# Kernel tuning notes

Measured on AMD Instinct MI355X. Metric: run time of the kernel, lower is better.

Reference implementation:

```python
import jax, jax.numpy as jnp
from jax import lax
import numpy as np


def _conv4d(x, w, b, stride, padding):
    # Faithful 4D conv emulation: K temporal slices, each its own 3D conv.
    # x: [B,Ci,T,D,H,W]; w: [K,Co,Ci,k,k,k]; b: [K,Co] or None.
    # Quirk preserved: bias b[i] is added once per contributing temporal tap i
    # (the torch code accumulates full conv3d outputs including bias).
    B, Ci, T = x.shape[0], x.shape[1], x.shape[2]
    K = w.shape[0]
    O = (T + 2 * padding - K) // stride + 1
    out = None
    for i in range(K):
        j = np.arange(O) * stride + i - padding          # static input frame idx per output frame
        valid = (j >= 0) & (j < T)
        jc = np.clip(j, 0, T - 1)
        xg = jnp.moveaxis(x[:, :, jc], 2, 1)             # [B,O,Ci,D,H,W]
        xg = xg.reshape(B * O, Ci, x.shape[3], x.shape[4], x.shape[5])
        y = lax.conv_general_dilated(xg, w[i], (stride,) * 3, [(padding, padding)] * 3,
                                     dimension_numbers=('NCDHW', 'OIDHW', 'NCDHW'))
        if b is not None:
            y = y + b[i][None, :, None, None, None]
        y = y.reshape(B, O, y.shape[1], y.shape[2], y.shape[3], y.shape[4])
        y = y * jnp.asarray(valid, y.dtype)[None, :, None, None, None, None]
        out = y if out is None else out + y
    return jnp.moveaxis(out, 1, 2)                       # [B,Co,O,D',H',W']


def _maxpool4d(x, k, s, p):
    # pool3d-per-frame then pool1d over T == one 4D max pool (max commutes)
    return lax.reduce_window(x, jnp.array(-jnp.inf, x.dtype), lax.max,
                             (1, 1, k, k, k, k), (1, 1, s, s, s, s),
                             [(0, 0), (0, 0)] + [(p, p)] * 4)


def _avgpool4d_2(x):
    # avg-of-avgs over a full (2,2,2,2) window == 4D average
    s = lax.reduce_window(x, jnp.array(0.0, x.dtype), lax.add,
                          (1, 1, 2, 2, 2, 2), (1,) * 6, [(0, 0)] * 6)
    return s / jnp.asarray(16.0, x.dtype)


def _block(x, w1, b1, w2, b2, stride, dw):
    y = jax.nn.relu(_conv4d(x, w1, b1, stride, 1))
    y = _conv4d(y, w2, b2, 1, 1)
    res = x if dw is None else _conv4d(x, dw, None, stride, 0)
    return jax.nn.relu(y + res)


def _forward(x, conv1_w, l1_w1, l1_b1, l1_w2, l1_b2,
             l2_w1, l2_b1, l2_w2, l2_b2, l2_dw,
             l3_w1, l3_b1, l3_w2, l3_b2, l3_dw,
             l4_w1, l4_b1, l4_w2, l4_b2, l4_dw, fc_w, fc_b):
    h = x[:, None]                                       # [B,1,T,D,H,W]
    h = jax.nn.relu(_conv4d(h, conv1_w, None, 2, 3))     # 36 -> 18
    h = _maxpool4d(h, 3, 2, 1)                           # 18 -> 9
    h = _block(h, l1_w1, l1_b1, l1_w2, l1_b2, 1, None)   # 9
    h = _block(h, l2_w1, l2_b1, l2_w2, l2_b2, 2, l2_dw)  # 9 -> 5
    h = _block(h, l3_w1, l3_b1, l3_w2, l3_b2, 2, l3_dw)  # 5 -> 3
    h = _block(h, l4_w1, l4_b1, l4_w2, l4_b2, 2, l4_dw)  # 3 -> 2
    h = _avgpool4d_2(h)                                  # 2 -> 1
    h = h.reshape(-1, 512)
    return h @ fc_w.T + fc_b


def setup_inputs() -> dict:
    key = jax.random.key(0)
    ks = jax.random.split(key, 40)
    ctr = iter(range(40))
    def w(shape, fan):
        return jax.random.normal(ks[next(ctr)], shape, jnp.float32) * np.float32(np.sqrt(2.0 / fan))
    def bias(shape):
        return jax.random.normal(ks[next(ctr)], shape, jnp.float32) * np.float32(0.01)
    d = {}
    d['x'] = jax.random.normal(ks[next(ctr)], (1, 36, 36, 36, 36), jnp.float32)
    d['conv1_w'] = w((7, 64, 1, 7, 7, 7), 343)
    d['l1_w1'] = w((3, 64, 64, 3, 3, 3), 64 * 27); d['l1_b1'] = bias((3, 64))
    d['l1_w2'] = w((3, 64, 64, 3, 3, 3), 64 * 27); d['l1_b2'] = bias((3, 64))
    d['l2_w1'] = w((3, 128, 64, 3, 3, 3), 64 * 27); d['l2_b1'] = bias((3, 128))
    d['l2_w2'] = w((3, 128, 128, 3, 3, 3), 128 * 27); d['l2_b2'] = bias((3, 128))
    d['l2_dw'] = w((1, 128, 64, 1, 1, 1), 64)
    d['l3_w1'] = w((3, 256, 128, 3, 3, 3), 128 * 27); d['l3_b1'] = bias((3, 256))
    d['l3_w2'] = w((3, 256, 256, 3, 3, 3), 256 * 27); d['l3_b2'] = bias((3, 256))
    d['l3_dw'] = w((1, 256, 128, 1, 1, 1), 128)
    d['l4_w1'] = w((3, 512, 256, 3, 3, 3), 256 * 27); d['l4_b1'] = bias((3, 512))
    d['l4_w2'] = w((3, 512, 512, 3, 3, 3), 512 * 27); d['l4_b2'] = bias((3, 512))
    d['l4_dw'] = w((1, 512, 256, 1, 1, 1), 256)
    d['fc_w'] = w((1, 512), 512); d['fc_b'] = bias((1,))
    return d


def reference(x, conv1_w, l1_w1, l1_b1, l1_w2, l1_b2,
              l2_w1, l2_b1, l2_w2, l2_b2, l2_dw,
              l3_w1, l3_b1, l3_w2, l3_b2, l3_dw,
              l4_w1, l4_b1, l4_w2, l4_b2, l4_dw, fc_w, fc_b):
    return _forward(x, conv1_w, l1_w1, l1_b1, l1_w2, l1_b2,
                    l2_w1, l2_b1, l2_w2, l2_b2, l2_dw,
                    l3_w1, l3_b1, l3_w2, l3_b2, l3_dw,
                    l4_w1, l4_b1, l4_w2, l4_b2, l4_dw, fc_w, fc_b)
```

## Files before the change

### kernel.cpp

```cpp
#include <hip/hip_runtime.h>

typedef __bf16 bf16x8 __attribute__((ext_vector_type(8)));
typedef float f32x4 __attribute__((ext_vector_type(4)));
typedef unsigned short ushortT;

__device__ __forceinline__ unsigned short f2bf(float f) {
    unsigned u = __float_as_uint(f);
    u += 0x7fffu + ((u >> 16) & 1u);
    return (unsigned short)(u >> 16);
}
__device__ __forceinline__ float bf2f(unsigned short h) {
    return __uint_as_float((unsigned)h << 16);
}

__global__ __launch_bounds__(256) void prep0(const float* __restrict__ x,
                                             const float* __restrict__ c1w,
                                             ushortT* __restrict__ xp,
                                             ushortT* __restrict__ o1) {
    int bid = blockIdx.x, tid = threadIdx.x;
    if (bid < 1737) {
        long idx = (long)bid * 256 + tid;
        if (idx >= 444528L) return;
        int q = (int)(idx % 6); long r = idx / 6;
        int h = (int)(r % 42); r /= 42;
        int d = (int)(r % 42); int t = (int)(r / 42);
        int tt = t - 3, dd = d - 3, hh = h - 3;
        bool rok = ((unsigned)tt < 36u) && ((unsigned)dd < 36u) && ((unsigned)hh < 36u);
        const float* src = x + (((long)tt * 36 + dd) * 36 + hh) * 36;
        union { ushortT s[8]; uint4 u; } v;
#pragma unroll
        for (int j = 0; j < 8; ++j) {
            int ww = q * 8 + j - 3;
            float f = (rok && (unsigned)ww < 36u) ? src[ww] : 0.f;
            v.s[j] = f2bf(f);
        }
        *(uint4*)(xp + idx * 8) = v.u;
    } else {
        int e = (bid - 1737) * 256 + tid;
        if (e < 200704) {
            int k = e % 3136, co = e / 3136;
            int kw = k & 7, kh = (k >> 3) & 7, kdt = k >> 6;
            int kt = kdt / 7, kd = kdt % 7;
            float v = 0.f;
            if (kh < 7 && kw < 7)
                v = c1w[(size_t)(kt * 64 + co) * 343 + kd * 49 + kh * 7 + kw];
            o1[e] = f2bf(v);
        }
    }
}

__global__ __launch_bounds__(128) void mega_kernel(
        const ushortT* __restrict__ xp, const ushortT* __restrict__ aw,
        ushortT* __restrict__ outc1,
        const float* __restrict__ w11, const float* __restrict__ w12,
        const float* __restrict__ w21, const float* __restrict__ w22,
        const float* __restrict__ w31, const float* __restrict__ w32,
        const float* __restrict__ w41, const float* __restrict__ w42,
        ushortT* __restrict__ o11, ushortT* __restrict__ o12,
        ushortT* __restrict__ o21, ushortT* __restrict__ o22,
        ushortT* __restrict__ o31, ushortT* __restrict__ o32,
        ushortT* __restrict__ o41, ushortT* __restrict__ o42) {
    __shared__ __align__(16) ushortT smem[8568];
    int bid = blockIdx.x, tid = threadIdx.x;

    if (bid < 1350) {
        int wt = bid % 5; int r = bid / 5;
        int ht = r % 5; r /= 5;
        int dt = r % 3; int ot = r / 3;
        int ow0 = wt * 4, oh0 = ht * 4, od0 = dt * 6;
        int gw0 = 2 * ow0, gh0 = 2 * oh0, gd0 = 2 * od0;

        int lane = tid & 63, wv = tid >> 6;
        int l15 = lane & 15, g = lane >> 4;
        int dh = l15 >> 2, dw = l15 & 3;

        const ushortT* ap0 = aw + (size_t)(wv * 32 + l15) * 3136 + g * 8;
        const ushortT* ap1 = ap0 + 16 * 3136;

        ushortT* curb = smem;
        ushortT* nxtb = smem + 4284;

        auto stage = [&](ushortT* buf, int kt) {
            int gt = 2 * ot + kt;
            for (int rr = tid; rr < 238; rr += 128) {
                int ld = rr / 14, lh = rr - ld * 14;
                const ushortT* s = xp +
                    ((size_t)((gt * 42 + gd0 + ld) * 42 + gh0 + lh)) * 48 + gw0;
                uint4 a = *(const uint4*)s;
                uint4 b = *(const uint4*)(s + 8);
                unsigned* d = (unsigned*)buf + rr * 9;
                d[0] = a.x; d[1] = a.y; d[2] = a.z; d[3] = a.w;
                d[4] = b.x; d[5] = b.y; d[6] = b.z; d[7] = b.w;
            }
        };

        f32x4 acc[2][6];
#pragma unroll
        for (int c = 0; c < 2; ++c)
#pragma unroll
            for (int m = 0; m < 6; ++m) acc[c][m] = (f32x4){0.f, 0.f, 0.f, 0.f};

        stage(curb, 0);
        __syncthreads();

        int lhl = (2 * dh + g) * 18 + 2 * dw;
        int kidx = 0;
        for (int kt = 0; kt < 7; ++kt) {
            if (kt < 6) stage(nxtb, kt + 1);
            for (int kd = 0; kd < 7; ++kd) {
                int C0 = kd * 252 + lhl;
#pragma unroll
                for (int khq = 0; khq < 2; ++khq) {
                    bf16x8 a0 = *(const bf16x8*)(ap0 + kidx);
                    bf16x8 a1 = *(const bf16x8*)(ap1 + kidx);
                    kidx += 32;
                    int C = C0 + khq * 72;
#pragma unroll
                    for (int m = 0; m < 6; ++m) {
                        int off = C + m * 504;
                        union { unsigned u[4]; bf16x8 v; } bb;
                        bb.u[0] = *(const unsigned*)(curb + off);
                        bb.u[1] = *(const unsigned*)(curb + off + 2);
                        bb.u[2] = *(const unsigned*)(curb + off + 4);
                        bb.u[3] = *(const unsigned*)(curb + off + 6);
                        acc[0][m] = __builtin_amdgcn_mfma_f32_16x16x32_bf16(a0, bb.v, acc[0][m], 0, 0, 0);
                        acc[1][m] = __builtin_amdgcn_mfma_f32_16x16x32_bf16(a1, bb.v, acc[1][m], 0, 0, 0);
                    }
                }
            }
            __syncthreads();
            ushortT* t2 = curb; curb = nxtb; nxtb = t2;
        }

        int oh = oh0 + dh, ow = ow0 + dw;
        if (oh < 18 && ow < 18) {
#pragma unroll
            for (int m = 0; m < 6; ++m) {
                int od = od0 + m;
                int pos = ((ot * 18 + od) * 18 + oh) * 18 + ow;
#pragma unroll
                for (int c = 0; c < 2; ++c) {
                    ushort4 st;
                    st.x = f2bf(fmaxf(acc[c][m][0], 0.f));
                    st.y = f2bf(fmaxf(acc[c][m][1], 0.f));
                    st.z = f2bf(fmaxf(acc[c][m][2], 0.f));
                    st.w = f2bf(fmaxf(acc[c][m][3], 0.f));
                    *(ushort4*)(outc1 + (size_t)pos * 64 + wv * 32 + c * 16 + g * 4) = st;
                }
            }
        }
        return;
    }

    int wb = bid - 1350;
    const float* in; ushortT* out; int Ci, Co, nc, base;
    if (wb < 1536) {
        if (wb < 384) {
            if (wb < 192) { in = w11; out = o11; Ci = 64; Co = 64; nc = 1; base = 0; }
            else          { in = w12; out = o12; Ci = 64; Co = 64; nc = 1; base = 192; }
        } else if (wb < 768) { in = w21; out = o21; Ci = 64;  Co = 128; nc = 1; base = 384; }
        else                 { in = w22; out = o22; Ci = 128; Co = 128; nc = 2; base = 768; }
    } else if (wb < 6144) {
        if (wb < 3072) { in = w31; out = o31; Ci = 128; Co = 256; nc = 2; base = 1536; }
        else           { in = w32; out = o32; Ci = 256; Co = 256; nc = 4; base = 3072; }
    } else {
        if (wb < 12288) { in = w41; out = o41; Ci = 256; Co = 512; nc = 4; base = 6144; }
        else            { in = w42; out = o42; Ci = 512; Co = 512; nc = 8; base = 12288; }
    }
    int lb = wb - base;
    int c64 = lb % nc;
    int co = (lb / nc) % Co;
    int i = lb / (nc * Co);

    const float* src = in + ((size_t)(i * Co + co) * Ci + 64 * c64) * 27;
    float* tile = (float*)smem;
    for (int e = tid; e < 432; e += 128)
        *(float4*)(tile + 4 * e) = *(const float4*)(src + 4 * e);
    __syncthreads();

    size_t nCb = Co >> 4, nKb = Ci >> 5;
    int cb = co >> 4, l15 = co & 15;
    for (int e = tid; e < 216; e += 128) {
        int tap = e >> 3, q8 = e & 7;
        int kb = 2 * c64 + (q8 >> 2);
        int g = q8 & 3;
        int tapP = i * 27 + tap;
        union { ushortT s[8]; uint4 u; } v;
#pragma unroll
        for (int j = 0; j < 8; ++j)
            v.s[j] = f2bf(tile[(q8 * 8 + j) * 27 + tap]);
        *(uint4*)(out + (((size_t)tapP * nCb + cb) * nKb + kb) * 512 + (g * 16 + l15) * 8) = v.u;
    }
}

__global__ void maxpool2(const ushortT* __restrict__ in, ushortT* __restrict__ out,
                         ushortT* __restrict__ zb) {
    int idx = blockIdx.x * 256 + threadIdx.x;
    if (idx < 128) zb[idx] = 0;
    if (idx >= 6561 * 16) return;
    int c4 = idx & 15;
    int p = idx >> 4;
    int ow = p % 9; int t = p / 9;
    int oh = t % 9; t /= 9;
    int od = t % 9; int ot = t / 9;
    ushort4 m = {0, 0, 0, 0};
    for (int kt = 0; kt < 3; ++kt) { int it = 2 * ot + kt - 1; if ((unsigned)it >= 18u) continue;
        for (int kd = 0; kd < 3; ++kd) { int id = 2 * od + kd - 1; if ((unsigned)id >= 18u) continue;
            for (int kh = 0; kh < 3; ++kh) { int ih = 2 * oh + kh - 1; if ((unsigned)ih >= 18u) continue;
                int rb = ((it * 18 + id) * 18 + ih) * 18;
                for (int kw = 0; kw < 3; ++kw) { int iw = 2 * ow + kw - 1; if ((unsigned)iw >= 18u) continue;
                    ushort4 v = *(const ushort4*)(in + (size_t)(rb + iw) * 64 + c4 * 4);
                    m.x = v.x > m.x ? v.x : m.x;
                    m.y = v.y > m.y ? v.y : m.y;
                    m.z = v.z > m.z ? v.z : m.z;
                    m.w = v.w > m.w ? v.w : m.w;
                }
            }
        }
    }
    *(ushort4*)(out + (size_t)p * 64 + c4 * 4) = m;
}

template <int KC, int FUSE, int TS>
__global__ void convmfma(const ushortT* __restrict__ xb, const ushortT* __restrict__ wt,
                         const float* __restrict__ bias, const ushortT* __restrict__ res,
                         ushortT* __restrict__ outb, float* __restrict__ part,
                         const ushortT* __restrict__ zq,
                         int Ci, int Co, int T, int O, int stride, int chunk,
                         const float* __restrict__ dwW, ushortT* __restrict__ dwOut) {
    if (dwW && blockIdx.y == (unsigned)(Co >> 6)) {
        int O2 = O * O, O3 = O2 * O, O4 = O3 * O;
        int total = Co * O4;
        int sthr = gridDim.x * gridDim.z * 256;
        for (int idx = (blockIdx.z * gridDim.x + blockIdx.x) * 256 + threadIdx.x;
             idx < total; idx += sthr) {
            int co = idx % Co;
            int pos = idx / Co;
            int ow = pos % O, oh = (pos / O) % O, od = (pos / O2) % O, ot = pos / O3;
            int ip = (((2 * ot) * T + 2 * od) * T + 2 * oh) * T + 2 * ow;
            const ushortT* xpp = xb + (size_t)ip * Ci;
            const float* wp = dwW + (size_t)co * Ci;
            float acc = 0.f;
            for (int c8 = 0; c8 < Ci; c8 += 8) {
                uint4 xv = *(const uint4*)(xpp + c8);
                float4 w0 = *(const float4*)(wp + c8);
                float4 w1 = *(const float4*)(wp + c8 + 4);
                acc = fmaf(bf2f((unsigned short)(xv.x & 0xffff)), w0.x, acc);
                acc = fmaf(bf2f((unsigned short)(xv.x >> 16)),    w0.y, acc);
                acc = fmaf(bf2f((unsigned short)(xv.y & 0xffff)), w0.z, acc);
                acc = fmaf(bf2f((unsigned short)(xv.y >> 16)),    w0.w, acc);
                acc = fmaf(bf2f((unsigned short)(xv.z & 0xffff)), w1.x, acc);
                acc = fmaf(bf2f((unsigned short)(xv.z >> 16)),    w1.y, acc);
                acc = fmaf(bf2f((unsigned short)(xv.w & 0xffff)), w1.z, acc);
                acc = fmaf(bf2f((unsigned short)(xv.w >> 16)),    w1.w, acc);
            }
            dwOut[idx] = f2bf(acc);
        }
        return;
    }

    int lane = threadIdx.x & 63;
    int wv = threadIdx.x >> 6;
    int p0 = blockIdx.x * 16;
    int cb = blockIdx.y * 4 + wv;
    int co0 = cb * 16;
    int zz = blockIdx.z;
    int ks, ts;
    if (TS > 1) { ks = zz / TS; ts = zz % TS; } else { ks = zz; ts = 0; }
    int cbase = ks * chunk;
    int kb0 = cbase >> 5;
    size_t nCb = Co >> 4, nKb = Ci >> 5;

    int pn = p0 + (lane & 15);
    int O2 = O * O, O3 = O2 * O, O4 = O3 * O;
    bool pv = pn < O4;
    int pc = pv ? pn : 0;
    int ow = pc % O, oh = (pc / O) % O, od = (pc / O2) % O, ot = pc / O3;
    int g = lane >> 4;
    int kl = cbase + g * 8;

    const ushortT* zp = zq + g * 8;

    f32x4 acc[4];
#pragma unroll
    for (int a = 0; a < 4; ++a) acc[a] = (f32x4){0.f, 0.f, 0.f, 0.f};

    int itb = ot * stride - 1, idb = od * stride - 1, ihb = oh * stride - 1, iwb = ow * stride - 1;

    if (TS == 1) {
#pragma unroll
        for (int i = 0; i < 3; ++i) {
            int it = itb + i;
            bool vt = pv && ((unsigned)it < (unsigned)T);
#pragma unroll
            for (int kd = 0; kd < 3; ++kd) {
                int id = idb + kd;
                bool vdd = vt && ((unsigned)id < (unsigned)T);
                int btd = (it * T + id) * T;
#pragma unroll
                for (int kh = 0; kh < 3; ++kh) {
                    int ih = ihb + kh;
                    bool vh = vdd && ((unsigned)ih < (unsigned)T);
#pragma unroll
                    for (int kw = 0; kw < 3; ++kw) {
                        int iw = iwb + kw;
                        bool v = vh && ((unsigned)iw < (unsigned)T);
                        int ip = (btd + ih) * T + iw;
                        const int tap = (i * 9 + kd * 3 + kh) * 3 + kw;
                        const ushortT* bp = v ? (xb + (size_t)ip * Ci + kl) : zp;
                        const ushortT* ap = wt + (((size_t)tap * nCb + cb) * nKb + kb0) * 512
                                            + lane * 8;
#pragma unroll
                        for (int kc = 0; kc < KC; ++kc) {
                            bf16x8 av = *(const bf16x8*)(ap + kc * 512);
                            bf16x8 bv = *(const bf16x8*)(bp + kc * 32);
                            acc[(tap * KC + kc) & 3] =
                                __builtin_amdgcn_mfma_f32_16x16x32_bf16(av, bv,
                                    acc[(tap * KC + kc) & 3], 0, 0, 0);
                        }
                    }
                }
            }
        }
    } else {
        int i = ts / 3, kd = ts % 3;
        int it = itb + i;
        int id = idb + kd;
        bool vt = pv && ((unsigned)it < (unsigned)T) && ((unsigned)id < (unsigned)T);
        int btd = (it * T + id) * T;
        int tapb = i * 27 + kd * 9;
#pragma unroll
        for (int kh = 0; kh < 3; ++kh) {
            int ih = ihb + kh;
            bool vh = vt && ((unsigned)ih < (unsigned)T);
#pragma unroll
            for (int kw = 0; kw < 3; ++kw) {
                int iw = iwb + kw;
                bool v = vh && ((unsigned)iw < (unsigned)T);
                int ip = (btd + ih) * T + iw;
                int tap = tapb + kh * 3 + kw;
                const ushortT* bp = v ? (xb + (size_t)ip * Ci + kl) : zp;
                const ushortT* ap = wt + (((size_t)tap * nCb + cb) * nKb + kb0) * 512
                                    + lane * 8;
#pragma unroll
                for (int kc = 0; kc < KC; ++kc) {
                    bf16x8 av = *(const bf16x8*)(ap + kc * 512);
                    bf16x8 bv = *(const bf16x8*)(bp + kc * 32);
                    acc[(kh * 3 + kw + kc) & 3] =
                        __builtin_amdgcn_mfma_f32_16x16x32_bf16(av, bv,
                            acc[(kh * 3 + kw + kc) & 3], 0, 0, 0);
                }
            }
        }
    }

    if (!pv) return;
    f32x4 asum;
#pragma unroll
    for (int r = 0; r < 4; ++r)
        asum[r] = (acc[0][r] + acc[1][r]) + (acc[2][r] + acc[3][r]);
    int cob = co0 + g * 4;
    if (FUSE) {
        float bb[4] = {0.f, 0.f, 0.f, 0.f};
        for (int i = 0; i < 3; ++i) {
            int it = itb + i;
            if ((unsigned)it < (unsigned)T) {
#pragma unroll
                for (int rr = 0; rr < 4; ++rr) bb[rr] += bias[i * Co + cob + rr];
            }
        }
        float rv[4] = {0.f, 0.f, 0.f, 0.f};
        if (res) {
            ushort4 r4 = *(const ushort4*)(res + (size_t)pn * Co + cob);
            rv[0] = bf2f(r4.x); rv[1] = bf2f(r4.y); rv[2] = bf2f(r4.z); rv[3] = bf2f(r4.w);
        }
        ushort4 st;
        st.x = f2bf(fmaxf(asum[0] + bb[0] + rv[0], 0.f));
        st.y = f2bf(fmaxf(asum[1] + bb[1] + rv[1], 0.f));
        st.z = f2bf(fmaxf(asum[2] + bb[2] + rv[2], 0.f));
        st.w = f2bf(fmaxf(asum[3] + bb[3] + rv[3], 0.f));
        *(ushort4*)(outb + (size_t)pn * Co + cob) = st;
    } else {
        *(f32x4*)(part + ((size_t)zz * O4 + pn) * Co + cob) = asum;
    }
}

__global__ void finalize_k(const float* __restrict__ part, int KS,
                           const float* __restrict__ bias, const ushortT* __restrict__ res,
                           ushortT* __restrict__ outb, int Co, int O4, int T, int O, int stride,
                           int total) {
    int idx = blockIdx.x * 256 + threadIdx.x;
    if (idx >= total) return;
    int co = idx % Co;
    int pos = idx / Co;
    float v = 0.f;
    for (int z = 0; z < KS; ++z) v += part[((size_t)z * O4 + pos) * Co + co];
    int ot = pos / (O * O * O);
    for (int i = 0; i < 3; ++i) {
        int it = ot * stride + i - 1;
        if ((unsigned)it < (unsigned)T) v += bias[i * Co + co];
    }
    if (res) v += bf2f(res[idx]);
    outb[idx] = f2bf(fmaxf(v, 0.f));
}

__global__ void avgfc2(const ushortT* __restrict__ xin, const float* __restrict__ fw,
                       const float* __restrict__ fb, float* __restrict__ out) {
    __shared__ float ls[8];
    int t = threadIdx.x;
    float s = 0.f;
#pragma unroll
    for (int pp = 0; pp < 16; ++pp) s += bf2f(xin[pp * 512 + t]);
    s = s * (1.f / 16.f) * fw[t];
    for (int off = 32; off > 0; off >>= 1) s += __shfl_xor(s, off, 64);
    if ((t & 63) == 0) ls[t >> 6] = s;
    __syncthreads();
    if (t == 0) {
        float tot = 0.f;
#pragma unroll
        for (int i = 0; i < 8; ++i) tot += ls[i];
        out[0] = tot + fb[0];
    }
}

extern "C" void kernel_launch(void* const* d_in, const int* in_sizes, int n_in,
                              void* d_out, int out_size, void* d_ws, size_t ws_size,
                              hipStream_t stream) {
    const float* x       = (const float*)d_in[0];
    const float* conv1_w = (const float*)d_in[1];
    const float* l1_w1 = (const float*)d_in[2];
    const float* l1_b1 = (const float*)d_in[3];
    const float* l1_w2 = (const float*)d_in[4];
    const float* l1_b2 = (const float*)d_in[5];
    const float* l2_w1 = (const float*)d_in[6];
    const float* l2_b1 = (const float*)d_in[7];
    const float* l2_w2 = (const float*)d_in[8];
    const float* l2_b2 = (const float*)d_in[9];
    const float* l2_dw = (const float*)d_in[10];
    const float* l3_w1 = (const float*)d_in[11];
    const float* l3_b1 = (const float*)d_in[12];
    const float* l3_w2 = (const float*)d_in[13];
    const float* l3_b2 = (const float*)d_in[14];
    const float* l3_dw = (const float*)d_in[15];
    const float* l4_w1 = (const float*)d_in[16];
    const float* l4_b1 = (const float*)d_in[17];
    const float* l4_w2 = (const float*)d_in[18];
    const float* l4_b2 = (const float*)d_in[19];
    const float* l4_dw = (const float*)d_in[20];
    const float* fc_w  = (const float*)d_in[21];
    const float* fc_b  = (const float*)d_in[22];
    float* outp = (float*)d_out;

    char* bp = (char*)d_ws;
    auto alloc = [&](size_t bytes) {
        char* r = bp;
        bp += (bytes + 255) & ~(size_t)255;
        return (void*)r;
    };
    ushortT* A16 = (ushortT*)alloc(6718464ull * 2);
    ushortT* XP  = (ushortT*)alloc(3556224ull * 2);
    ushortT* Aw1 = (ushortT*)alloc(200704ull * 2);
    ushortT* X0 = (ushortT*)alloc(419904ull * 2);
    ushortT* Y1 = (ushortT*)alloc(419904ull * 2);
    ushortT* X1 = (ushortT*)alloc(419904ull * 2);
    ushortT* Y2 = (ushortT*)alloc(80000ull * 2);
    ushortT* R2 = (ushortT*)alloc(80000ull * 2);
    ushortT* X2 = (ushortT*)alloc(80000ull * 2);
    ushortT* Y3 = (ushortT*)alloc(20736ull * 2);
    ushortT* R3 = (ushortT*)alloc(20736ull * 2);
    ushortT* X3 = (ushortT*)alloc(20736ull * 2);
    ushortT* Y4 = (ushortT*)alloc(8192ull * 2);
    ushortT* R4 = (ushortT*)alloc(8192ull * 2);
    ushortT* X4 = (ushortT*)alloc(8192ull * 2);
    ushortT* W11 = (ushortT*)alloc(331776ull * 2);
    ushortT* W12 = (ushortT*)alloc(331776ull * 2);
    ushortT* W21 = (ushortT*)alloc(663552ull * 2);
    ushortT* W22 = (ushortT*)alloc(1327104ull * 2);
    ushortT* W31 = (ushortT*)alloc(2654208ull * 2);
    ushortT* W32 = (ushortT*)alloc(5308416ull * 2);
    ushortT* W41 = (ushortT*)alloc(10616832ull * 2);
    ushortT* W42 = (ushortT*)alloc(21233664ull * 2);
    float* P    = (float*)alloc(1492992ull * 4);
    ushortT* ZB = (ushortT*)alloc(256);
    if ((size_t)(bp - (char*)d_ws) > ws_size) return;

    prep0<<<2521, 256, 0, stream>>>(x, conv1_w, XP, Aw1);

    mega_kernel<<<25926, 128, 0, stream>>>(XP, Aw1, A16,
                                           l1_w1, l1_w2, l2_w1, l2_w2, l3_w1, l3_w2,
                                           l4_w1, l4_w2,
                                           W11, W12, W21, W22, W31, W32, W41, W42);

    maxpool2<<<411, 256, 0, stream>>>(A16, X0, ZB);

    convmfma<2, 1, 1><<<dim3(411, 1, 1), 256, 0, stream>>>(
        X0, W11, l1_b1, nullptr, Y1, nullptr, ZB, 64, 64, 9, 9, 1, 64, nullptr, nullptr);
    convmfma<2, 1, 1><<<dim3(411, 1, 1), 256, 0, stream>>>(
        Y1, W12, l1_b2, X0, X1, nullptr, ZB, 64, 64, 9, 9, 1, 64, nullptr, nullptr);

    convmfma<2, 1, 1><<<dim3(40, 3, 1), 256, 0, stream>>>(
        X1, W21, l2_b1, nullptr, Y2, nullptr, ZB, 64, 128, 9, 5, 2, 64, l2_dw, R2);
    convmfma<4, 1, 1><<<dim3(40, 2, 1), 256, 0, stream>>>(
        Y2, W22, l2_b2, R2, X2, nullptr, ZB, 128, 128, 5, 5, 1, 128, nullptr, nullptr);

    convmfma<1, 0, 9><<<dim3(6, 5, 36), 256, 0, stream>>>(
        X2, W31, nullptr, nullptr, nullptr, P, ZB, 128, 256, 5, 3, 2, 32, l3_dw, R3);
    finalize_k<<<81, 256, 0, stream>>>(P, 36, l3_b1, nullptr, Y3, 256, 81, 5, 3, 2, 20736);
    convmfma<1, 0, 9><<<dim3(6, 4, 72), 256, 0, stream>>>(
        Y3, W32, nullptr, nullptr, nullptr, P, ZB, 256, 256, 3, 3, 1, 32, nullptr, nullptr);
    finalize_k<<<81, 256, 0, stream>>>(P, 72, l3_b2, R3, X3, 256, 81, 3, 3, 1, 20736);

    convmfma<1, 0, 9><<<dim3(1, 9, 72), 256, 0, stream>>>(
        X3, W41, nullptr, nullptr, nullptr, P, ZB, 256, 512, 3, 2, 2, 32, l4_dw, R4);
    finalize_k<<<32, 256, 0, stream>>>(P, 72, l4_b1, nullptr, Y4, 512, 16, 3, 2, 2, 8192);
    convmfma<1, 0, 9><<<dim3(1, 8, 144), 256, 0, stream>>>(
        Y4, W42, nullptr, nullptr, nullptr, P, ZB, 512, 512, 2, 2, 1, 32, nullptr, nullptr);
    finalize_k<<<32, 256, 0, stream>>>(P, 144, l4_b2, R4, X4, 512, 16, 2, 2, 1, 8192);

    avgfc2<<<1, 512, 0, stream>>>(X4, fc_w, fc_b, outp);
}
```

Baseline: 481.0 us.

## Move weight repacking into prep kernel with coarser tiles; pad conv1 LDS rows

The fp32-to-bf16 weight repacking for all residual layers moves out of the conv1 mega kernel and into the prep kernel. It now uses one 256-thread block per 16x32 output tile staged through a ~55KB LDS tile, replacing many tiny 128-thread blocks that each handled one output channel slice. The conv1 kernel now launches only its 1350 compute blocks, and its staged-input LDS row stride grows from 9 to 13 dwords, likely to reduce bank conflicts. Costs are larger LDS per block in both kernels, which lowers occupancy, and the conv1 compute can no longer overlap with the weight repacking.

Measured after the change: 500.7 us. 1.04x slower.

```diff
diff --git a/kernel.cpp b/kernel.cpp
--- a/kernel.cpp
+++ b/kernel.cpp
@@ -15,8 +15,17 @@
 
 __global__ __launch_bounds__(256) void prep0(const float* __restrict__ x,
                                              const float* __restrict__ c1w,
+                                             const float* __restrict__ w11, const float* __restrict__ w12,
+                                             const float* __restrict__ w21, const float* __restrict__ w22,
+                                             const float* __restrict__ w31, const float* __restrict__ w32,
+                                             const float* __restrict__ w41, const float* __restrict__ w42,
                                              ushortT* __restrict__ xp,
-                                             ushortT* __restrict__ o1) {
+                                             ushortT* __restrict__ o1,
+                                             ushortT* __restrict__ o11, ushortT* __restrict__ o12,
+                                             ushortT* __restrict__ o21, ushortT* __restrict__ o22,
+                                             ushortT* __restrict__ o31, ushortT* __restrict__ o32,
+                                             ushortT* __restrict__ o41, ushortT* __restrict__ o42) {
+    __shared__ float tile[13936];
     int bid = blockIdx.x, tid = threadIdx.x;
     if (bid < 1737) {
         long idx = (long)bid * 256 + tid;
@@ -35,7 +44,9 @@
             v.s[j] = f2bf(f);
         }
         *(uint4*)(xp + idx * 8) = v.u;
-    } else {
+        return;
+    }
+    if (bid < 2521) {
         int e = (bid - 1737) * 256 + tid;
         if (e < 200704) {
             int k = e % 3136, co = e / 3136;
@@ -46,150 +57,140 @@
                 v = c1w[(size_t)(kt * 64 + co) * 343 + kd * 49 + kh * 7 + kw];
             o1[e] = f2bf(v);
         }
+        return;
+    }
+
+    int wb = bid - 2521;
+    const float* in; ushortT* out; int Ci, Co;
+    int base;
+    if (wb < 192) {
+        if (wb < 48) {
+            if (wb < 24) { in = w11; out = o11; Ci = 64; Co = 64; base = 0; }
+            else         { in = w12; out = o12; Ci = 64; Co = 64; base = 24; }
+        } else if (wb < 96) { in = w21; out = o21; Ci = 64;  Co = 128; base = 48; }
+        else                { in = w22; out = o22; Ci = 128; Co = 128; base = 96; }
+    } else if (wb < 768) {
+        if (wb < 384) { in = w31; out = o31; Ci = 128; Co = 256; base = 192; }
+        else          { in = w32; out = o32; Ci = 256; Co = 256; base = 384; }
+    } else {
+        if (wb < 1536) { in = w41; out = o41; Ci = 256; Co = 512; base = 768; }
+        else           { in = w42; out = o42; Ci = 512; Co = 512; base = 1536; }
+    }
+    int lb = wb - base;
+    int nCb = Co >> 4, nKb = Ci >> 5;
+    int per_i = nCb * nKb;
+    int i = lb / per_i;
+    int r2 = lb - i * per_i;
+    int cb = r2 / nKb, kb = r2 - cb * nKb;
+
+    const float* src0 = in + ((size_t)(i * Co + cb * 16) * Ci + kb * 32) * 27;
+    size_t costride = (size_t)Ci * 27;
+    for (int e = tid; e < 3456; e += 256) {
+        int cl = e / 216, q = e - cl * 216;
+        *(float4*)(tile + cl * 871 + 4 * q) = *(const float4*)(src0 + cl * costride + 4 * q);
+    }
+    __syncthreads();
+    for (int e = tid; e < 1728; e += 256) {
+        int tap = e >> 6, widx = e & 63;
+        int l15 = widx & 15, g = widx >> 4;
+        union { ushortT s[8]; uint4 u; } v;
+#pragma unroll
+        for (int j = 0; j < 8; ++j)
+            v.s[j] = f2bf(tile[l15 * 871 + (g * 8 + j) * 27 + tap]);
+        *(uint4*)(out + (((size_t)(i * 27 + tap) * nCb + cb) * nKb + kb) * 512 + widx * 8) = v.u;
     }
 }
 
 __global__ __launch_bounds__(128) void mega_kernel(
         const ushortT* __restrict__ xp, const ushortT* __restrict__ aw,
-        ushortT* __restrict__ outc1,
-        const float* __restrict__ w11, const float* __restrict__ w12,
-        const float* __restrict__ w21, const float* __restrict__ w22,
-        const float* __restrict__ w31, const float* __restrict__ w32,
-        const float* __restrict__ w41, const float* __restrict__ w42,
-        ushortT* __restrict__ o11, ushortT* __restrict__ o12,
-        ushortT* __restrict__ o21, ushortT* __restrict__ o22,
-        ushortT* __restrict__ o31, ushortT* __restrict__ o32,
-        ushortT* __restrict__ o41, ushortT* __restrict__ o42) {
-    __shared__ __align__(16) ushortT smem[8568];
+        ushortT* __restrict__ outc1) {
+    __shared__ __align__(16) ushortT smem[12376];
     int bid = blockIdx.x, tid = threadIdx.x;
 
-    if (bid < 1350) {
-        int wt = bid % 5; int r = bid / 5;
-        int ht = r % 5; r /= 5;
-        int dt = r % 3; int ot = r / 3;
-        int ow0 = wt * 4, oh0 = ht * 4, od0 = dt * 6;
-        int gw0 = 2 * ow0, gh0 = 2 * oh0, gd0 = 2 * od0;
-
-        int lane = tid & 63, wv = tid >> 6;
-        int l15 = lane & 15, g = lane >> 4;
-        int dh = l15 >> 2, dw = l15 & 3;
-
-        const ushortT* ap0 = aw + (size_t)(wv * 32 + l15) * 3136 + g * 8;
-        const ushortT* ap1 = ap0 + 16 * 3136;
-
-        ushortT* curb = smem;
-        ushortT* nxtb = smem + 4284;
-
-        auto stage = [&](ushortT* buf, int kt) {
-            int gt = 2 * ot + kt;
-            for (int rr = tid; rr < 238; rr += 128) {
-                int ld = rr / 14, lh = rr - ld * 14;
-                const ushortT* s = xp +
-                    ((size_t)((gt * 42 + gd0 + ld) * 42 + gh0 + lh)) * 48 + gw0;
-                uint4 a = *(const uint4*)s;
-                uint4 b = *(const uint4*)(s + 8);
-                unsigned* d = (unsigned*)buf + rr * 9;
-                d[0] = a.x; d[1] = a.y; d[2] = a.z; d[3] = a.w;
-                d[4] = b.x; d[5] = b.y; d[6] = b.z; d[7] = b.w;
-            }
-        };
-
-        f32x4 acc[2][6];
-#pragma unroll
-        for (int c = 0; c < 2; ++c)
-#pragma unroll
-            for (int m = 0; m < 6; ++m) acc[c][m] = (f32x4){0.f, 0.f, 0.f, 0.f};
-
-        stage(curb, 0);
+    int wt = bid % 5; int r = bid / 5;
+    int ht = r % 5; r /= 5;
+    int dt = r % 3; int ot = r / 3;
+    int ow0 = wt * 4, oh0 = ht * 4, od0 = dt * 6;
+    int gw0 = 2 * ow0, gh0 = 2 * oh0, gd0 = 2 * od0;
+
+    int lane = tid & 63, wv = tid >> 6;
+    int l15 = lane & 15, g = lane >> 4;
+    int dh = l15 >> 2, dw = l15 & 3;
+
+    const ushortT* ap0 = aw + (size_t)(wv * 32 + l15) * 3136 + g * 8;
+    const ushortT* ap1 = ap0 + 16 * 3136;
+
+    ushortT* curb = smem;
+    ushortT* nxtb = smem + 6188;
+
+    auto stage = [&](ushortT* buf, int kt) {
+        int gt = 2 * ot + kt;
+        for (int rr = tid; rr < 238; rr += 128) {
+            int ld = rr / 14, lh = rr - ld * 14;
+            const ushortT* s = xp +
+                ((size_t)((gt * 42 + gd0 + ld) * 42 + gh0 + lh)) * 48 + gw0;
+            uint4 a = *(const uint4*)s;
+            uint4 b = *(const uint4*)(s + 8);
+            unsigned* d = (unsigned*)buf + rr * 13;
+            d[0] = a.x; d[1] = a.y; d[2] = a.z; d[3] = a.w;
+            d[4] = b.x; d[5] = b.y; d[6] = b.z; d[7] = b.w;
+        }
+    };
+
+    f32x4 acc[2][6];
+#pragma unroll
+    for (int c = 0; c < 2; ++c)
+#pragma unroll
+        for (int m = 0; m < 6; ++m) acc[c][m] = (f32x4){0.f, 0.f, 0.f, 0.f};
+
+    stage(curb, 0);
+    __syncthreads();
+
+    int lhl = (2 * dh + g) * 26 + 2 * dw;
+    int kidx = 0;
+    for (int kt = 0; kt < 7; ++kt) {
+        if (kt < 6) stage(nxtb, kt + 1);
+        for (int kd = 0; kd < 7; ++kd) {
+            int C0 = kd * 364 + lhl;
+#pragma unroll
+            for (int khq = 0; khq < 2; ++khq) {
+                bf16x8 a0 = *(const bf16x8*)(ap0 + kidx);
+                bf16x8 a1 = *(const bf16x8*)(ap1 + kidx);
+                kidx += 32;
+                int C = C0 + khq * 104;
+#pragma unroll
+                for (int m = 0; m < 6; ++m) {
+                    int off = C + m * 728;
+                    union { unsigned u[4]; bf16x8 v; } bb;
+                    bb.u[0] = *(const unsigned*)(curb + off);
+                    bb.u[1] = *(const unsigned*)(curb + off + 2);
+                    bb.u[2] = *(const unsigned*)(curb + off + 4);
+                    bb.u[3] = *(const unsigned*)(curb + off + 6);
+                    acc[0][m] = __builtin_amdgcn_mfma_f32_16x16x32_bf16(a0, bb.v, acc[0][m], 0, 0, 0);
+                    acc[1][m] = __builtin_amdgcn_mfma_f32_16x16x32_bf16(a1, bb.v, acc[1][m], 0, 0, 0);
+                }
+            }
+        }
         __syncthreads();
-
-        int lhl = (2 * dh + g) * 18 + 2 * dw;
-        int kidx = 0;
-        for (int kt = 0; kt < 7; ++kt) {
-            if (kt < 6) stage(nxtb, kt + 1);
-            for (int kd = 0; kd < 7; ++kd) {
-                int C0 = kd * 252 + lhl;
-#pragma unroll
-                for (int khq = 0; khq < 2; ++khq) {
-                    bf16x8 a0 = *(const bf16x8*)(ap0 + kidx);
-                    bf16x8 a1 = *(const bf16x8*)(ap1 + kidx);
-                    kidx += 32;
-                    int C = C0 + khq * 72;
-#pragma unroll
-                    for (int m = 0; m < 6; ++m) {
-                        int off = C + m * 504;
-                        union { unsigned u[4]; bf16x8 v; } bb;
-                        bb.u[0] = *(const unsigned*)(curb + off);
-                        bb.u[1] = *(const unsigned*)(curb + off + 2);
-                        bb.u[2] = *(const unsigned*)(curb + off + 4);
-                        bb.u[3] = *(const unsigned*)(curb + off + 6);
-                        acc[0][m] = __builtin_amdgcn_mfma_f32_16x16x32_bf16(a0, bb.v, acc[0][m], 0, 0, 0);
-                        acc[1][m] = __builtin_amdgcn_mfma_f32_16x16x32_bf16(a1, bb.v, acc[1][m], 0, 0, 0);
-                    }
-                }
-            }
-            __syncthreads();
-            ushortT* t2 = curb; curb = nxtb; nxtb = t2;
-        }
-
-        int oh = oh0 + dh, ow = ow0 + dw;
-        if (oh < 18 && ow < 18) {
-#pragma unroll
-            for (int m = 0; m < 6; ++m) {
-                int od = od0 + m;
-                int pos = ((ot * 18 + od) * 18 + oh) * 18 + ow;
-#pragma unroll
-                for (int c = 0; c < 2; ++c) {
-                    ushort4 st;
-                    st.x = f2bf(fmaxf(acc[c][m][0], 0.f));
-                    st.y = f2bf(fmaxf(acc[c][m][1], 0.f));
-                    st.z = f2bf(fmaxf(acc[c][m][2], 0.f));
-                    st.w = f2bf(fmaxf(acc[c][m][3], 0.f));
-                    *(ushort4*)(outc1 + (size_t)pos * 64 + wv * 32 + c * 16 + g * 4) = st;
-                }
-            }
-        }
-        return;
-    }
-
-    int wb = bid - 1350;
-    const float* in; ushortT* out; int Ci, Co, nc, base;
-    if (wb < 1536) {
-        if (wb < 384) {
-            if (wb < 192) { in = w11; out = o11; Ci = 64; Co = 64; nc = 1; base = 0; }
-            else          { in = w12; out = o12; Ci = 64; Co = 64; nc = 1; base = 192; }
-        } else if (wb < 768) { in = w21; out = o21; Ci = 64;  Co = 128; nc = 1; base = 384; }
-        else                 { in = w22; out = o22; Ci = 128; Co = 128; nc = 2; base = 768; }
-    } else if (wb < 6144) {
-        if (wb < 3072) { in = w31; out = o31; Ci = 128; Co = 256; nc = 2; base = 1536; }
-        else           { in = w32; out = o32; Ci = 256; Co = 256; nc = 4; base = 3072; }
-    } else {
-        if (wb < 12288) { in = w41; out = o41; Ci = 256; Co = 512; nc = 4; base = 6144; }
-        else            { in = w42; out = o42; Ci = 512; Co = 512; nc = 8; base = 12288; }
-    }
-    int lb = wb - base;
-    int c64 = lb % nc;
-    int co = (lb / nc) % Co;
-    int i = lb / (nc * Co);
-
-    const float* src = in + ((size_t)(i * Co + co) * Ci + 64 * c64) * 27;
-    float* tile = (float*)smem;
-    for (int e = tid; e < 432; e += 128)
-        *(float4*)(tile + 4 * e) = *(const float4*)(src + 4 * e);
-    __syncthreads();
-
-    size_t nCb = Co >> 4, nKb = Ci >> 5;
-    int cb = co >> 4, l15 = co & 15;
-    for (int e = tid; e < 216; e += 128) {
-        int tap = e >> 3, q8 = e & 7;
-        int kb = 2 * c64 + (q8 >> 2);
-        int g = q8 & 3;
-        int tapP = i * 27 + tap;
-        union { ushortT s[8]; uint4 u; } v;
-#pragma unroll
-        for (int j = 0; j < 8; ++j)
-            v.s[j] = f2bf(tile[(q8 * 8 + j) * 27 + tap]);
-        *(uint4*)(out + (((size_t)tapP * nCb + cb) * nKb + kb) * 512 + (g * 16 + l15) * 8) = v.u;
+        ushortT* t2 = curb; curb = nxtb; nxtb = t2;
+    }
+
+    int oh = oh0 + dh, ow = ow0 + dw;
+    if (oh < 18 && ow < 18) {
+#pragma unroll
+        for (int m = 0; m < 6; ++m) {
+            int od = od0 + m;
+            int pos = ((ot * 18 + od) * 18 + oh) * 18 + ow;
+#pragma unroll
+            for (int c = 0; c < 2; ++c) {
+                ushort4 st;
+                st.x = f2bf(fmaxf(acc[c][m][0], 0.f));
+                st.y = f2bf(fmaxf(acc[c][m][1], 0.f));
+                st.z = f2bf(fmaxf(acc[c][m][2], 0.f));
+                st.w = f2bf(fmaxf(acc[c][m][3], 0.f));
+                *(ushort4*)(outc1 + (size_t)pos * 64 + wv * 32 + c * 16 + g * 4) = st;
+            }
+        }
     }
 }
 
@@ -484,12 +485,12 @@
     ushortT* ZB = (ushortT*)alloc(256);
     if ((size_t)(bp - (char*)d_ws) > ws_size) return;
 
-    prep0<<<2521, 256, 0, stream>>>(x, conv1_w, XP, Aw1);
-
-    mega_kernel<<<25926, 128, 0, stream>>>(XP, Aw1, A16,
-                                           l1_w1, l1_w2, l2_w1, l2_w2, l3_w1, l3_w2,
-                                           l4_w1, l4_w2,
-                                           W11, W12, W21, W22, W31, W32, W41, W42);
+    prep0<<<5593, 256, 0, stream>>>(x, conv1_w,
+                                    l1_w1, l1_w2, l2_w1, l2_w2, l3_w1, l3_w2, l4_w1, l4_w2,
+                                    XP, Aw1,
+                                    W11, W12, W21, W22, W31, W32, W41, W42);
+
+    mega_kernel<<<1350, 128, 0, stream>>>(XP, Aw1, A16);
 
     maxpool2<<<411, 256, 0, stream>>>(A16, X0, ZB);
 
```
